# Performance work log

Hardware: AMD Instinct MI355X
Metric: run time of the kernel (lower is better)

## Reference

```python
import jax, jax.numpy as jnp
import numpy as np

D_MODEL = 1024
N_HEADS = 16
DEPTH = D_MODEL // N_HEADS
P_FEAT = 64
NEG_BIG = -1.0e9


def setup_inputs() -> dict:
    key = jax.random.key(0)
    ks = jax.random.split(key, 12)
    B, S = 4, 2048
    s = 1.0 / np.sqrt(D_MODEL)
    return {
        "q": jax.random.normal(ks[0], (B, S, D_MODEL), jnp.float32),
        "k": jax.random.normal(ks[1], (B, S, D_MODEL), jnp.float32),
        "v": jax.random.normal(ks[2], (B, S, D_MODEL), jnp.float32),
        "protocol_features": jax.random.normal(ks[3], (B, P_FEAT), jnp.float32),
        "mask": jax.random.randint(ks[4], (B, 1, 1, S), 0, 2).astype(jnp.float32),
        "wq": jax.random.normal(ks[5], (D_MODEL, D_MODEL), jnp.float32) * s,
        "bq": jnp.zeros((D_MODEL,), jnp.float32),
        "wk": jax.random.normal(ks[6], (D_MODEL, D_MODEL), jnp.float32) * s,
        "bk": jnp.zeros((D_MODEL,), jnp.float32),
        "wv": jax.random.normal(ks[7], (D_MODEL, D_MODEL), jnp.float32) * s,
        "bv": jnp.zeros((D_MODEL,), jnp.float32),
        "wg": jax.random.normal(ks[8], (P_FEAT, N_HEADS), jnp.float32) * (1.0 / np.sqrt(P_FEAT)),
        "bg": jnp.zeros((N_HEADS,), jnp.float32),
    }


def _split_heads(x, B):
    # [B,S,d_model] -> [B,H,S,depth]
    return x.reshape(B, -1, N_HEADS, DEPTH).transpose(0, 2, 1, 3)


def reference(q, k, v, protocol_features, mask, wq, bq, wk, bk, wv, bv, wg, bg):
    B = q.shape[0]
    qh = _split_heads(q @ wq + bq, B)
    kh = _split_heads(k @ wk + bk, B)
    vh = _split_heads(v @ wv + bv, B)
    # scaled QK^T: [B,H,S,S]
    logits = jnp.einsum("bhqd,bhkd->bhqk", qh, kh) / jnp.sqrt(jnp.float32(DEPTH))
    # per-head protocol gate (sigmoid), broadcast over q/k positions
    validity = jax.nn.sigmoid(protocol_features @ wg + bg)  # [B,H]
    logits = logits * validity[:, :, None, None]
    logits = logits + mask * NEG_BIG
    attn = jax.nn.softmax(logits, axis=-1)
    out = jnp.einsum("bhqk,bhkd->bhqd", attn, vh)
    concat = out.transpose(0, 2, 1, 3).reshape(B, -1, D_MODEL)
    return concat, attn
```

## Files before the change

kernel.cpp:

```cpp
#include <hip/hip_runtime.h>

#define S_LEN 2048
#define NB 4
#define NH 16
#define BHN 64
#define DM 1024
#define DEP 64
#define MROWS 8192

typedef __attribute__((ext_vector_type(8))) short short8;
typedef __attribute__((ext_vector_type(4))) float f32x4;

#define MFMA_BF16(a, b, c) __builtin_amdgcn_mfma_f32_16x16x32_bf16((a), (b), (c), 0, 0, 0)

typedef __attribute__((address_space(1))) const void* as1cv;
typedef __attribute__((address_space(3))) void* as3v;

__device__ __forceinline__ void gld16(const void* g, void* l) {
  __builtin_amdgcn_global_load_lds((as1cv)g, (as3v)l, 16, 0, 0);
}

__device__ __forceinline__ unsigned short f2bf(float f) {
  unsigned u = __float_as_uint(f);
  u += 0x7fffu + ((u >> 16) & 1u);
  return (unsigned short)(u >> 16);
}

__device__ __forceinline__ unsigned cvtpk(float a, float b) {
  unsigned r;
  asm("v_cvt_pk_bf16_f32 %0, %1, %2" : "=v"(r) : "v"(a), "v"(b));
  return r;
}

__device__ __forceinline__ int SWZ(int row, int gran) {
  return row * 64 + ((gran ^ (row & 7)) << 3);
}

__global__ void gate_kernel(const float* __restrict__ pf, const float* __restrict__ wg,
                            const float* __restrict__ bg, float* __restrict__ validity) {
  int t = threadIdx.x;
  int b = t >> 4, h = t & 15;
  float s = bg[h];
  for (int i = 0; i < 64; i++) s += pf[b * 64 + i] * wg[i * NH + h];
  validity[t] = 1.0f / (1.0f + __expf(-s));
}

__global__ __launch_bounds__(256) void conv_bf16_kernel(const float* __restrict__ in,
                                                        unsigned short* __restrict__ out) {
  size_t i = ((size_t)blockIdx.x * 256 + threadIdx.x) * 8;
  float4 a = *(const float4*)(in + i);
  float4 b = *(const float4*)(in + i + 4);
  union { unsigned short us[8]; uint4 v; } o;
  o.us[0] = f2bf(a.x); o.us[1] = f2bf(a.y); o.us[2] = f2bf(a.z); o.us[3] = f2bf(a.w);
  o.us[4] = f2bf(b.x); o.us[5] = f2bf(b.y); o.us[6] = f2bf(b.z); o.us[7] = f2bf(b.w);
  *(uint4*)(out + i) = o.v;
}

__global__ __launch_bounds__(256) void wt_kernel(const float* __restrict__ W,
                                                 unsigned short* __restrict__ Wt) {
  __shared__ unsigned short T[64][72];
  int k0 = blockIdx.x * 64, n0 = blockIdx.y * 64;
  int t = threadIdx.x;
  int r = t >> 2, c4 = (t & 3) * 16;
  for (int j = 0; j < 16; j += 4) {
    float4 v = *(const float4*)&W[(size_t)(k0 + r) * DM + n0 + c4 + j];
    T[r][c4 + j + 0] = f2bf(v.x); T[r][c4 + j + 1] = f2bf(v.y);
    T[r][c4 + j + 2] = f2bf(v.z); T[r][c4 + j + 3] = f2bf(v.w);
  }
  __syncthreads();
  union { unsigned short us[16]; uint4 v[2]; } o;
  for (int j = 0; j < 16; j++) o.us[j] = T[c4 + j][r];
  *(uint4*)&Wt[(size_t)(n0 + r) * DM + k0 + c4] = o.v[0];
  *(uint4*)&Wt[(size_t)(n0 + r) * DM + k0 + c4 + 8] = o.v[1];
}

__global__ __launch_bounds__(256) void vt_kernel(const unsigned short* __restrict__ vh,
                                                 unsigned short* __restrict__ vhT) {
  __shared__ unsigned short T[64][72];
  int bh = blockIdx.y;
  int s0 = blockIdx.x * 64;
  int t = threadIdx.x;
  int r = t >> 2, c4 = (t & 3) * 16;
  const unsigned short* src = vh + ((size_t)bh * S_LEN + s0 + r) * DEP + c4;
  *(uint4*)&T[r][c4] = *(const uint4*)src;
  *(uint4*)&T[r][c4 + 8] = *(const uint4*)(src + 8);
  __syncthreads();
  union { unsigned short us[16]; uint4 v[2]; } o;
  for (int j = 0; j < 16; j++) o.us[j] = T[c4 + j][r];
  unsigned short* dst = vhT + ((size_t)bh * DEP + r) * S_LEN + s0 + c4;
  *(uint4*)dst = o.v[0];
  *(uint4*)(dst + 8) = o.v[1];
}

__global__ __launch_bounds__(256) void proj_gemm(const unsigned short* __restrict__ A,
                                                 const unsigned short* __restrict__ Bt,
                                                 const float* __restrict__ bias,
                                                 unsigned short* __restrict__ Y) {
  __shared__ unsigned short As[128 * 64], Bs[128 * 64];
  const int K = DM;
  int tid = threadIdx.x, w = tid >> 6, l = tid & 63, g = l >> 4, lc = l & 15;
  int r0 = blockIdx.x * 128, c0 = blockIdx.y * 128;
  int wr = w >> 1, wc = w & 1;
  int lrow = l >> 3, lcol = (l & 7) * 8;
  f32x4 acc[4][4] = {};
  for (int k0 = 0; k0 < K; k0 += 64) {
    __syncthreads();
    for (int i = 0; i < 4; i++) {
      int row = (w * 4 + i) * 8 + lrow;
      gld16(A + (size_t)(r0 + row) * K + k0 + lcol, &As[(w * 4 + i) * 512]);
      gld16(Bt + (size_t)(c0 + row) * K + k0 + lcol, &Bs[(w * 4 + i) * 512]);
    }
    __syncthreads();
    for (int kk = 0; kk < 2; kk++) {
      short8 a[4], b[4];
      for (int m = 0; m < 4; m++)
        a[m] = *(const short8*)&As[(wr * 64 + m * 16 + lc) * 64 + kk * 32 + g * 8];
      for (int n = 0; n < 4; n++)
        b[n] = *(const short8*)&Bs[(wc * 64 + n * 16 + lc) * 64 + kk * 32 + g * 8];
      for (int m = 0; m < 4; m++)
        for (int n = 0; n < 4; n++)
          acc[m][n] = MFMA_BF16(a[m], b[n], acc[m][n]);
    }
  }
  for (int n = 0; n < 4; n++) {
    int c = c0 + wc * 64 + n * 16 + lc;
    float bi = bias[c];
    int h = c >> 6, d = c & 63;
    for (int m = 0; m < 4; m++) {
      int rowbase = r0 + wr * 64 + m * 16 + g * 4;
      for (int r = 0; r < 4; r++) {
        int row = rowbase + r;
        int b_ = row >> 11, s = row & 2047;
        Y[(((size_t)b_ * NH + h) * S_LEN + s) * DEP + d] = f2bf(acc[m][n][r] + bi);
      }
    }
  }
}

__global__ __launch_bounds__(512) void attn_fused(const unsigned short* __restrict__ qh,
                                                  const unsigned short* __restrict__ kh,
                                                  const unsigned short* __restrict__ vhT,
                                                  const float* __restrict__ validity,
                                                  const float* __restrict__ mask,
                                                  float* __restrict__ concat,
                                                  float* __restrict__ attn) {
  __shared__ union {
    unsigned short Q[128 * 64];
    float PF[8][16 * 68];
  } QP;
  __shared__ unsigned short Ks[2][64 * 64], Vs[2][64 * 64];
  __shared__ float Ms[S_LEN];
  int bh = blockIdx.y, b = bh >> 4, h = bh & 15;
  int q0 = blockIdx.x * 128;
  int tid = threadIdx.x, w = tid >> 6, l = tid & 63, g = l >> 4, lc = l & 15;
  int srow = l >> 3;
  int sgran = (l & 7) ^ srow;
  float scale = validity[bh] * 0.125f * 1.44269504f;
  for (int i = tid; i < S_LEN; i += 512)
    Ms[i] = mask[(size_t)b * S_LEN + i] * (-1.44269504e9f);

  const unsigned short* qb = qh + (size_t)bh * S_LEN * DEP;
  const unsigned short* kb = kh + (size_t)bh * S_LEN * DEP;
  const unsigned short* vb = vhT + (size_t)bh * DEP * S_LEN;

  for (int i = 0; i < 2; i++)
    gld16(qb + (size_t)(q0 + i * 64 + w * 8 + srow) * DEP + sgran * 8,
          &QP.Q[(i * 64 + w * 8) * 64]);
  gld16(kb + (size_t)(w * 8 + srow) * DEP + sgran * 8, &Ks[0][w * 512]);
  __syncthreads();

  int qrow = w * 16 + lc;
  short8 aq0 = *(const short8*)&QP.Q[SWZ(qrow, g)];
  short8 aq1 = *(const short8*)&QP.Q[SWZ(qrow, 4 + g)];

  float ell[4] = {0.f, 0.f, 0.f, 0.f};
#pragma unroll 2
  for (int kt = 0; kt < 32; kt++) {
    const int cb = kt & 1;
    if (kt < 31)
      gld16(kb + (size_t)((kt + 1) * 64 + w * 8 + srow) * DEP + sgran * 8,
            &Ks[cb ^ 1][w * 512]);
    __builtin_amdgcn_sched_barrier(0);
    if (kt < 31) { asm volatile("s_waitcnt vmcnt(1)" ::: "memory"); }
    else         { asm volatile("s_waitcnt vmcnt(0)" ::: "memory"); }
    __builtin_amdgcn_sched_barrier(0);
    for (int f = 0; f < 4; f++) {
      int krow = f * 16 + lc;
      short8 b0 = *(const short8*)&Ks[cb][SWZ(krow, g)];
      short8 b1 = *(const short8*)&Ks[cb][SWZ(krow, 4 + g)];
      f32x4 c = {};
      __builtin_amdgcn_s_setprio(1);
      c = MFMA_BF16(aq0, b0, c);
      c = MFMA_BF16(aq1, b1, c);
      __builtin_amdgcn_s_setprio(0);
      float mb = Ms[kt * 64 + f * 16 + lc];
      for (int r = 0; r < 4; r++) ell[r] += exp2f(fmaf(c[r], scale, mb));
    }
    __builtin_amdgcn_s_barrier();
  }
  for (int m = 8; m >= 1; m >>= 1)
    for (int r = 0; r < 4; r++) ell[r] += __shfl_xor(ell[r], m, 64);
  float rinv[4];
  for (int r = 0; r < 4; r++) rinv[r] = 1.0f / ell[r];

  gld16(kb + (size_t)(w * 8 + srow) * DEP + sgran * 8, &Ks[0][w * 512]);
  gld16(vb + (size_t)(w * 8 + srow) * S_LEN + sgran * 8, &Vs[0][w * 512]);
  __syncthreads();

  float* PFw = QP.PF[w];
  float* arow2 = attn + ((size_t)bh * S_LEN + q0 + w * 16 + lc) * S_LEN + g * 8;

  f32x4 O[4] = {};
#pragma unroll 2
  for (int kt = 0; kt < 32; kt++) {
    const int cb = kt & 1;
    if (kt < 31) {
      gld16(kb + (size_t)((kt + 1) * 64 + w * 8 + srow) * DEP + sgran * 8,
            &Ks[cb ^ 1][w * 512]);
      gld16(vb + (size_t)(w * 8 + srow) * S_LEN + (kt + 1) * 64 + sgran * 8,
            &Vs[cb ^ 1][w * 512]);
    }
    __builtin_amdgcn_sched_barrier(0);
    if (kt < 31) { asm volatile("s_waitcnt vmcnt(6)" ::: "memory"); }
    else         { asm volatile("s_waitcnt vmcnt(4)" ::: "memory"); }
    __builtin_amdgcn_sched_barrier(0);
    for (int f = 0; f < 4; f++) {
      int krow = f * 16 + lc;
      short8 b0 = *(const short8*)&Ks[cb][SWZ(krow, g)];
      short8 b1 = *(const short8*)&Ks[cb][SWZ(krow, 4 + g)];
      f32x4 c = {};
      __builtin_amdgcn_s_setprio(1);
      c = MFMA_BF16(aq0, b0, c);
      c = MFMA_BF16(aq1, b1, c);
      __builtin_amdgcn_s_setprio(0);
      float mb = Ms[kt * 64 + f * 16 + lc];
      for (int r = 0; r < 4; r++) {
        float p = exp2f(fmaf(c[r], scale, mb)) * rinv[r];
        PFw[(g * 4 + r) * 68 + f * 16 + lc] = p;
      }
    }
    f32x4 t0 = *(const f32x4*)&PFw[lc * 68 + g * 8];
    f32x4 t1 = *(const f32x4*)&PFw[lc * 68 + g * 8 + 4];
    f32x4 t2 = *(const f32x4*)&PFw[lc * 68 + 32 + g * 8];
    f32x4 t3 = *(const f32x4*)&PFw[lc * 68 + 32 + g * 8 + 4];
    union { uint4 u; short8 s; } pk0, pk1;
    pk0.u = uint4{cvtpk(t0[0], t0[1]), cvtpk(t0[2], t0[3]),
                  cvtpk(t1[0], t1[1]), cvtpk(t1[2], t1[3])};
    pk1.u = uint4{cvtpk(t2[0], t2[1]), cvtpk(t2[2], t2[3]),
                  cvtpk(t3[0], t3[1]), cvtpk(t3[2], t3[3])};
    *(f32x4*)(arow2 + kt * 64) = t0;
    *(f32x4*)(arow2 + kt * 64 + 4) = t1;
    *(f32x4*)(arow2 + kt * 64 + 32) = t2;
    *(f32x4*)(arow2 + kt * 64 + 36) = t3;
    __builtin_amdgcn_s_setprio(1);
    for (int n = 0; n < 4; n++) {
      int vrow = n * 16 + lc;
      short8 v0 = *(const short8*)&Vs[cb][SWZ(vrow, g)];
      short8 v1 = *(const short8*)&Vs[cb][SWZ(vrow, 4 + g)];
      O[n] = MFMA_BF16(pk0.s, v0, O[n]);
      O[n] = MFMA_BF16(pk1.s, v1, O[n]);
    }
    __builtin_amdgcn_s_setprio(0);
    __builtin_amdgcn_s_barrier();
  }
  for (int n = 0; n < 4; n++)
    for (int r = 0; r < 4; r++)
      concat[((size_t)b * S_LEN + q0 + w * 16 + g * 4 + r) * DM + h * DEP + n * 16 + lc] =
          O[n][r];
}

extern "C" void kernel_launch(void* const* d_in, const int* in_sizes, int n_in,
                              void* d_out, int out_size, void* d_ws, size_t ws_size,
                              hipStream_t stream) {
  const float* q    = (const float*)d_in[0];
  const float* k    = (const float*)d_in[1];
  const float* v    = (const float*)d_in[2];
  const float* pf   = (const float*)d_in[3];
  const float* mask = (const float*)d_in[4];
  const float* wq   = (const float*)d_in[5];
  const float* bq   = (const float*)d_in[6];
  const float* wk   = (const float*)d_in[7];
  const float* bk   = (const float*)d_in[8];
  const float* wv   = (const float*)d_in[9];
  const float* bv   = (const float*)d_in[10];
  const float* wg   = (const float*)d_in[11];
  const float* bg   = (const float*)d_in[12];

  float* concat = (float*)d_out;
  float* attn   = concat + (size_t)NB * S_LEN * DM;

  unsigned short* qbf = (unsigned short*)attn;
  unsigned short* kbf = qbf + (size_t)MROWS * DM;
  unsigned short* vbf = kbf + (size_t)MROWS * DM;
  unsigned short* wqT = vbf + (size_t)MROWS * DM;
  unsigned short* wkT = wqT + (size_t)DM * DM;
  unsigned short* wvT = wkT + (size_t)DM * DM;

  float* validity = (float*)d_ws;
  unsigned short* qhp = (unsigned short*)((char*)d_ws + 4096);
  unsigned short* khp = qhp + (size_t)MROWS * DM;
  unsigned short* vhp = khp + (size_t)MROWS * DM;
  unsigned short* vhT = vhp + (size_t)MROWS * DM;

  gate_kernel<<<1, 64, 0, stream>>>(pf, wg, bg, validity);

  conv_bf16_kernel<<<4096, 256, 0, stream>>>(q, qbf);
  conv_bf16_kernel<<<4096, 256, 0, stream>>>(k, kbf);
  conv_bf16_kernel<<<4096, 256, 0, stream>>>(v, vbf);

  wt_kernel<<<dim3(16, 16), 256, 0, stream>>>(wq, wqT);
  wt_kernel<<<dim3(16, 16), 256, 0, stream>>>(wk, wkT);
  wt_kernel<<<dim3(16, 16), 256, 0, stream>>>(wv, wvT);

  proj_gemm<<<dim3(64, 8), 256, 0, stream>>>(qbf, wqT, bq, qhp);
  proj_gemm<<<dim3(64, 8), 256, 0, stream>>>(kbf, wkT, bk, khp);
  proj_gemm<<<dim3(64, 8), 256, 0, stream>>>(vbf, wvT, bv, vhp);

  vt_kernel<<<dim3(32, 64), 256, 0, stream>>>(vhp, vhT);

  attn_fused<<<dim3(16, 64), 512, 0, stream>>>(qhp, khp, vhT, validity, mask, concat, attn);
}
```

Before: 536.8 us.

## Process two query tiles per block, fusing second tile's row-sum pass into first's output pass

Each block now handles 256 query rows as two 128-row tiles, and the grid is halved. The denominator pass for tile B is folded into tile A's output pass, so K is streamed three times per two tiles instead of four. This removes one K sweep and its QK^T recompute per pair of tiles. In exchange the grid shrinks to 512 blocks, which lowers parallelism on a many-CU GPU, and per-thread register pressure rises.

```diff
diff --git a/kernel.cpp b/kernel.cpp
--- a/kernel.cpp
+++ b/kernel.cpp
@@ -151,7 +151,7 @@
   __shared__ unsigned short Ks[2][64 * 64], Vs[2][64 * 64];
   __shared__ float Ms[S_LEN];
   int bh = blockIdx.y, b = bh >> 4, h = bh & 15;
-  int q0 = blockIdx.x * 128;
+  int q0A = blockIdx.x * 256, q0B = q0A + 128;
   int tid = threadIdx.x, w = tid >> 6, l = tid & 63, g = l >> 4, lc = l & 15;
   int srow = l >> 3;
   int sgran = (l & 7) ^ srow;
@@ -162,18 +162,17 @@
   const unsigned short* qb = qh + (size_t)bh * S_LEN * DEP;
   const unsigned short* kb = kh + (size_t)bh * S_LEN * DEP;
   const unsigned short* vb = vhT + (size_t)bh * DEP * S_LEN;
+  int qrow = w * 16 + lc;
 
   for (int i = 0; i < 2; i++)
-    gld16(qb + (size_t)(q0 + i * 64 + w * 8 + srow) * DEP + sgran * 8,
+    gld16(qb + (size_t)(q0A + i * 64 + w * 8 + srow) * DEP + sgran * 8,
           &QP.Q[(i * 64 + w * 8) * 64]);
   gld16(kb + (size_t)(w * 8 + srow) * DEP + sgran * 8, &Ks[0][w * 512]);
   __syncthreads();
-
-  int qrow = w * 16 + lc;
-  short8 aq0 = *(const short8*)&QP.Q[SWZ(qrow, g)];
-  short8 aq1 = *(const short8*)&QP.Q[SWZ(qrow, 4 + g)];
-
-  float ell[4] = {0.f, 0.f, 0.f, 0.f};
+  short8 aqA0 = *(const short8*)&QP.Q[SWZ(qrow, g)];
+  short8 aqA1 = *(const short8*)&QP.Q[SWZ(qrow, 4 + g)];
+
+  float ellA[4] = {0.f, 0.f, 0.f, 0.f};
 #pragma unroll 2
   for (int kt = 0; kt < 32; kt++) {
     const int cb = kt & 1;
@@ -190,26 +189,32 @@
       short8 b1 = *(const short8*)&Ks[cb][SWZ(krow, 4 + g)];
       f32x4 c = {};
       __builtin_amdgcn_s_setprio(1);
-      c = MFMA_BF16(aq0, b0, c);
-      c = MFMA_BF16(aq1, b1, c);
+      c = MFMA_BF16(aqA0, b0, c);
+      c = MFMA_BF16(aqA1, b1, c);
       __builtin_amdgcn_s_setprio(0);
       float mb = Ms[kt * 64 + f * 16 + lc];
-      for (int r = 0; r < 4; r++) ell[r] += exp2f(fmaf(c[r], scale, mb));
+      for (int r = 0; r < 4; r++) ellA[r] += exp2f(fmaf(c[r], scale, mb));
     }
     __builtin_amdgcn_s_barrier();
   }
   for (int m = 8; m >= 1; m >>= 1)
-    for (int r = 0; r < 4; r++) ell[r] += __shfl_xor(ell[r], m, 64);
-  float rinv[4];
-  for (int r = 0; r < 4; r++) rinv[r] = 1.0f / ell[r];
-
+    for (int r = 0; r < 4; r++) ellA[r] += __shfl_xor(ellA[r], m, 64);
+  float rinvA[4];
+  for (int r = 0; r < 4; r++) rinvA[r] = 1.0f / ellA[r];
+
+  for (int i = 0; i < 2; i++)
+    gld16(qb + (size_t)(q0B + i * 64 + w * 8 + srow) * DEP + sgran * 8,
+          &QP.Q[(i * 64 + w * 8) * 64]);
   gld16(kb + (size_t)(w * 8 + srow) * DEP + sgran * 8, &Ks[0][w * 512]);
   gld16(vb + (size_t)(w * 8 + srow) * S_LEN + sgran * 8, &Vs[0][w * 512]);
   __syncthreads();
+  short8 aqB0 = *(const short8*)&QP.Q[SWZ(qrow, g)];
+  short8 aqB1 = *(const short8*)&QP.Q[SWZ(qrow, 4 + g)];
+  __syncthreads();
 
   float* PFw = QP.PF[w];
-  float* arow2 = attn + ((size_t)bh * S_LEN + q0 + w * 16 + lc) * S_LEN + g * 8;
-
+  float* arowA = attn + ((size_t)bh * S_LEN + q0A + w * 16 + lc) * S_LEN + g * 8;
+  float ellB[4] = {0.f, 0.f, 0.f, 0.f};
   f32x4 O[4] = {};
 #pragma unroll 2
   for (int kt = 0; kt < 32; kt++) {
@@ -228,15 +233,18 @@
       int krow = f * 16 + lc;
       short8 b0 = *(const short8*)&Ks[cb][SWZ(krow, g)];
       short8 b1 = *(const short8*)&Ks[cb][SWZ(krow, 4 + g)];
-      f32x4 c = {};
+      f32x4 cA = {}, cB = {};
       __builtin_amdgcn_s_setprio(1);
-      c = MFMA_BF16(aq0, b0, c);
-      c = MFMA_BF16(aq1, b1, c);
+      cA = MFMA_BF16(aqA0, b0, cA);
+      cA = MFMA_BF16(aqA1, b1, cA);
+      cB = MFMA_BF16(aqB0, b0, cB);
+      cB = MFMA_BF16(aqB1, b1, cB);
       __builtin_amdgcn_s_setprio(0);
       float mb = Ms[kt * 64 + f * 16 + lc];
       for (int r = 0; r < 4; r++) {
-        float p = exp2f(fmaf(c[r], scale, mb)) * rinv[r];
-        PFw[(g * 4 + r) * 68 + f * 16 + lc] = p;
+        float pA = exp2f(fmaf(cA[r], scale, mb)) * rinvA[r];
+        PFw[(g * 4 + r) * 68 + f * 16 + lc] = pA;
+        ellB[r] += exp2f(fmaf(cB[r], scale, mb));
       }
     }
     f32x4 t0 = *(const f32x4*)&PFw[lc * 68 + g * 8];
@@ -248,10 +256,10 @@
                   cvtpk(t1[0], t1[1]), cvtpk(t1[2], t1[3])};
     pk1.u = uint4{cvtpk(t2[0], t2[1]), cvtpk(t2[2], t2[3]),
                   cvtpk(t3[0], t3[1]), cvtpk(t3[2], t3[3])};
-    *(f32x4*)(arow2 + kt * 64) = t0;
-    *(f32x4*)(arow2 + kt * 64 + 4) = t1;
-    *(f32x4*)(arow2 + kt * 64 + 32) = t2;
-    *(f32x4*)(arow2 + kt * 64 + 36) = t3;
+    *(f32x4*)(arowA + kt * 64) = t0;
+    *(f32x4*)(arowA + kt * 64 + 4) = t1;
+    *(f32x4*)(arowA + kt * 64 + 32) = t2;
+    *(f32x4*)(arowA + kt * 64 + 36) = t3;
     __builtin_amdgcn_s_setprio(1);
     for (int n = 0; n < 4; n++) {
       int vrow = n * 16 + lc;
@@ -265,8 +273,75 @@
   }
   for (int n = 0; n < 4; n++)
     for (int r = 0; r < 4; r++)
-      concat[((size_t)b * S_LEN + q0 + w * 16 + g * 4 + r) * DM + h * DEP + n * 16 + lc] =
+      concat[((size_t)b * S_LEN + q0A + w * 16 + g * 4 + r) * DM + h * DEP + n * 16 + lc] =
           O[n][r];
+  for (int m = 8; m >= 1; m >>= 1)
+    for (int r = 0; r < 4; r++) ellB[r] += __shfl_xor(ellB[r], m, 64);
+  float rinvB[4];
+  for (int r = 0; r < 4; r++) rinvB[r] = 1.0f / ellB[r];
+
+  gld16(kb + (size_t)(w * 8 + srow) * DEP + sgran * 8, &Ks[0][w * 512]);
+  gld16(vb + (size_t)(w * 8 + srow) * S_LEN + sgran * 8, &Vs[0][w * 512]);
+  __syncthreads();
+  float* arowB = attn + ((size_t)bh * S_LEN + q0B + w * 16 + lc) * S_LEN + g * 8;
+  f32x4 O2[4] = {{0.f, 0.f, 0.f, 0.f}, {0.f, 0.f, 0.f, 0.f},
+                 {0.f, 0.f, 0.f, 0.f}, {0.f, 0.f, 0.f, 0.f}};
+#pragma unroll 2
+  for (int kt = 0; kt < 32; kt++) {
+    const int cb = kt & 1;
+    if (kt < 31) {
+      gld16(kb + (size_t)((kt + 1) * 64 + w * 8 + srow) * DEP + sgran * 8,
+            &Ks[cb ^ 1][w * 512]);
+      gld16(vb + (size_t)(w * 8 + srow) * S_LEN + (kt + 1) * 64 + sgran * 8,
+            &Vs[cb ^ 1][w * 512]);
+    }
+    __builtin_amdgcn_sched_barrier(0);
+    if (kt < 31) { asm volatile("s_waitcnt vmcnt(6)" ::: "memory"); }
+    else         { asm volatile("s_waitcnt vmcnt(4)" ::: "memory"); }
+    __builtin_amdgcn_sched_barrier(0);
+    for (int f = 0; f < 4; f++) {
+      int krow = f * 16 + lc;
+      short8 b0 = *(const short8*)&Ks[cb][SWZ(krow, g)];
+      short8 b1 = *(const short8*)&Ks[cb][SWZ(krow, 4 + g)];
+      f32x4 c = {};
+      __builtin_amdgcn_s_setprio(1);
+      c = MFMA_BF16(aqB0, b0, c);
+      c = MFMA_BF16(aqB1, b1, c);
+      __builtin_amdgcn_s_setprio(0);
+      float mb = Ms[kt * 64 + f * 16 + lc];
+      for (int r = 0; r < 4; r++) {
+        float p = exp2f(fmaf(c[r], scale, mb)) * rinvB[r];
+        PFw[(g * 4 + r) * 68 + f * 16 + lc] = p;
+      }
+    }
+    f32x4 t0 = *(const f32x4*)&PFw[lc * 68 + g * 8];
+    f32x4 t1 = *(const f32x4*)&PFw[lc * 68 + g * 8 + 4];
+    f32x4 t2 = *(const f32x4*)&PFw[lc * 68 + 32 + g * 8];
+    f32x4 t3 = *(const f32x4*)&PFw[lc * 68 + 32 + g * 8 + 4];
+    union { uint4 u; short8 s; } pk0, pk1;
+    pk0.u = uint4{cvtpk(t0[0], t0[1]), cvtpk(t0[2], t0[3]),
+                  cvtpk(t1[0], t1[1]), cvtpk(t1[2], t1[3])};
+    pk1.u = uint4{cvtpk(t2[0], t2[1]), cvtpk(t2[2], t2[3]),
+                  cvtpk(t3[0], t3[1]), cvtpk(t3[2], t3[3])};
+    *(f32x4*)(arowB + kt * 64) = t0;
+    *(f32x4*)(arowB + kt * 64 + 4) = t1;
+    *(f32x4*)(arowB + kt * 64 + 32) = t2;
+    *(f32x4*)(arowB + kt * 64 + 36) = t3;
+    __builtin_amdgcn_s_setprio(1);
+    for (int n = 0; n < 4; n++) {
+      int vrow = n * 16 + lc;
+      short8 v0 = *(const short8*)&Vs[cb][SWZ(vrow, g)];
+      short8 v1 = *(const short8*)&Vs[cb][SWZ(vrow, 4 + g)];
+      O2[n] = MFMA_BF16(pk0.s, v0, O2[n]);
+      O2[n] = MFMA_BF16(pk1.s, v1, O2[n]);
+    }
+    __builtin_amdgcn_s_setprio(0);
+    __builtin_amdgcn_s_barrier();
+  }
+  for (int n = 0; n < 4; n++)
+    for (int r = 0; r < 4; r++)
+      concat[((size_t)b * S_LEN + q0B + w * 16 + g * 4 + r) * DM + h * DEP + n * 16 + lc] =
+          O2[n][r];
 }
 
 extern "C" void kernel_launch(void* const* d_in, const int* in_sizes, int n_in,
@@ -318,5 +393,5 @@
 
   vt_kernel<<<dim3(32, 64), 256, 0, stream>>>(vhp, vhT);
 
-  attn_fused<<<dim3(16, 64), 512, 0, stream>>>(qhp, khp, vhT, validity, mask, concat, attn);
-}
+  attn_fused<<<dim3(8, 64), 512, 0, stream>>>(qhp, khp, vhT, validity, mask, concat, attn);
+}
```

After: 591.9 us. 1.1x slower.

## Remap attention blocks per XCD and use 128-row K tiles in the row-sum pass

Applied to the files above, without the earlier changes.

Shared K and V buffers merge into one KV array so the first pass can load 128-row K tiles, halving its loop iterations and barriers. The grid is flattened to 1024 blocks and remapped so consecutive block IDs round-robin across the 8 XCDs. All q-tiles of a given batch-head then land on the same XCD and can share K/V in its L2. The risk is extra vmcnt tuning for the larger tile and a fixed XCD-count assumption in the mapping.

```diff
diff --git a/kernel.cpp b/kernel.cpp
--- a/kernel.cpp
+++ b/kernel.cpp
@@ -148,10 +148,15 @@
     unsigned short Q[128 * 64];
     float PF[8][16 * 68];
   } QP;
-  __shared__ unsigned short Ks[2][64 * 64], Vs[2][64 * 64];
+  __shared__ unsigned short KV[4][64 * 64];
   __shared__ float Ms[S_LEN];
-  int bh = blockIdx.y, b = bh >> 4, h = bh & 15;
-  int q0 = blockIdx.x * 128;
+
+  int id = blockIdx.x;
+  int cxcd = id & 7, j = id >> 3;
+  int bh = cxcd * 8 + (j >> 4);
+  int q0 = (j & 15) * 128;
+  int b = bh >> 4, h = bh & 15;
+
   int tid = threadIdx.x, w = tid >> 6, l = tid & 63, g = l >> 4, lc = l & 15;
   int srow = l >> 3;
   int sgran = (l & 7) ^ srow;
@@ -162,38 +167,44 @@
   const unsigned short* qb = qh + (size_t)bh * S_LEN * DEP;
   const unsigned short* kb = kh + (size_t)bh * S_LEN * DEP;
   const unsigned short* vb = vhT + (size_t)bh * DEP * S_LEN;
-
+  int qrow = w * 16 + lc;
+
+  unsigned short* B0 = &KV[0][0];
+  unsigned short* B1 = &KV[2][0];
   for (int i = 0; i < 2; i++)
     gld16(qb + (size_t)(q0 + i * 64 + w * 8 + srow) * DEP + sgran * 8,
           &QP.Q[(i * 64 + w * 8) * 64]);
-  gld16(kb + (size_t)(w * 8 + srow) * DEP + sgran * 8, &Ks[0][w * 512]);
+  for (int i = 0; i < 2; i++)
+    gld16(kb + (size_t)(i * 64 + w * 8 + srow) * DEP + sgran * 8,
+          B0 + (i * 64 + w * 8) * 64);
   __syncthreads();
-
-  int qrow = w * 16 + lc;
   short8 aq0 = *(const short8*)&QP.Q[SWZ(qrow, g)];
   short8 aq1 = *(const short8*)&QP.Q[SWZ(qrow, 4 + g)];
 
   float ell[4] = {0.f, 0.f, 0.f, 0.f};
-#pragma unroll 2
-  for (int kt = 0; kt < 32; kt++) {
-    const int cb = kt & 1;
-    if (kt < 31)
-      gld16(kb + (size_t)((kt + 1) * 64 + w * 8 + srow) * DEP + sgran * 8,
-            &Ks[cb ^ 1][w * 512]);
+  for (int kt2 = 0; kt2 < 16; kt2++) {
+    const int cb = kt2 & 1;
+    unsigned short* cur = cb ? B1 : B0;
+    if (kt2 < 15) {
+      unsigned short* nxt = cb ? B0 : B1;
+      for (int i = 0; i < 2; i++)
+        gld16(kb + (size_t)((kt2 + 1) * 128 + i * 64 + w * 8 + srow) * DEP + sgran * 8,
+              nxt + (i * 64 + w * 8) * 64);
+    }
     __builtin_amdgcn_sched_barrier(0);
-    if (kt < 31) { asm volatile("s_waitcnt vmcnt(1)" ::: "memory"); }
-    else         { asm volatile("s_waitcnt vmcnt(0)" ::: "memory"); }
+    if (kt2 < 15) { asm volatile("s_waitcnt vmcnt(2)" ::: "memory"); }
+    else          { asm volatile("s_waitcnt vmcnt(0)" ::: "memory"); }
     __builtin_amdgcn_sched_barrier(0);
-    for (int f = 0; f < 4; f++) {
+    for (int f = 0; f < 8; f++) {
       int krow = f * 16 + lc;
-      short8 b0 = *(const short8*)&Ks[cb][SWZ(krow, g)];
-      short8 b1 = *(const short8*)&Ks[cb][SWZ(krow, 4 + g)];
+      short8 b0 = *(const short8*)&cur[SWZ(krow, g)];
+      short8 b1 = *(const short8*)&cur[SWZ(krow, 4 + g)];
       f32x4 c = {};
       __builtin_amdgcn_s_setprio(1);
       c = MFMA_BF16(aq0, b0, c);
       c = MFMA_BF16(aq1, b1, c);
       __builtin_amdgcn_s_setprio(0);
-      float mb = Ms[kt * 64 + f * 16 + lc];
+      float mb = Ms[kt2 * 128 + f * 16 + lc];
       for (int r = 0; r < 4; r++) ell[r] += exp2f(fmaf(c[r], scale, mb));
     }
     __builtin_amdgcn_s_barrier();
@@ -203,8 +214,8 @@
   float rinv[4];
   for (int r = 0; r < 4; r++) rinv[r] = 1.0f / ell[r];
 
-  gld16(kb + (size_t)(w * 8 + srow) * DEP + sgran * 8, &Ks[0][w * 512]);
-  gld16(vb + (size_t)(w * 8 + srow) * S_LEN + sgran * 8, &Vs[0][w * 512]);
+  gld16(kb + (size_t)(w * 8 + srow) * DEP + sgran * 8, &KV[0][w * 512]);
+  gld16(vb + (size_t)(w * 8 + srow) * S_LEN + sgran * 8, &KV[2][w * 512]);
   __syncthreads();
 
   float* PFw = QP.PF[w];
@@ -216,9 +227,9 @@
     const int cb = kt & 1;
     if (kt < 31) {
       gld16(kb + (size_t)((kt + 1) * 64 + w * 8 + srow) * DEP + sgran * 8,
-            &Ks[cb ^ 1][w * 512]);
+            &KV[cb ^ 1][w * 512]);
       gld16(vb + (size_t)(w * 8 + srow) * S_LEN + (kt + 1) * 64 + sgran * 8,
-            &Vs[cb ^ 1][w * 512]);
+            &KV[2 + (cb ^ 1)][w * 512]);
     }
     __builtin_amdgcn_sched_barrier(0);
     if (kt < 31) { asm volatile("s_waitcnt vmcnt(6)" ::: "memory"); }
@@ -226,8 +237,8 @@
     __builtin_amdgcn_sched_barrier(0);
     for (int f = 0; f < 4; f++) {
       int krow = f * 16 + lc;
-      short8 b0 = *(const short8*)&Ks[cb][SWZ(krow, g)];
-      short8 b1 = *(const short8*)&Ks[cb][SWZ(krow, 4 + g)];
+      short8 b0 = *(const short8*)&KV[cb][SWZ(krow, g)];
+      short8 b1 = *(const short8*)&KV[cb][SWZ(krow, 4 + g)];
       f32x4 c = {};
       __builtin_amdgcn_s_setprio(1);
       c = MFMA_BF16(aq0, b0, c);
@@ -255,8 +266,8 @@
     __builtin_amdgcn_s_setprio(1);
     for (int n = 0; n < 4; n++) {
       int vrow = n * 16 + lc;
-      short8 v0 = *(const short8*)&Vs[cb][SWZ(vrow, g)];
-      short8 v1 = *(const short8*)&Vs[cb][SWZ(vrow, 4 + g)];
+      short8 v0 = *(const short8*)&KV[2 + cb][SWZ(vrow, g)];
+      short8 v1 = *(const short8*)&KV[2 + cb][SWZ(vrow, 4 + g)];
       O[n] = MFMA_BF16(pk0.s, v0, O[n]);
       O[n] = MFMA_BF16(pk1.s, v1, O[n]);
     }
@@ -318,5 +329,5 @@
 
   vt_kernel<<<dim3(32, 64), 256, 0, stream>>>(vhp, vhT);
 
-  attn_fused<<<dim3(16, 64), 512, 0, stream>>>(qhp, khp, vhT, validity, mask, concat, attn);
-}
+  attn_fused<<<1024, 512, 0, stream>>>(qhp, khp, vhT, validity, mask, concat, attn);
+}
```

Result: faster. 504.8 us (-6.0%).
